# Kernel optimization log

Measured on AMD Instinct MI355X. Metric: run time of the kernel, lower is better.

## Reference

```python
import jax, jax.numpy as jnp
import numpy as np

TEMPERATURE = 0.07
NORM_EPS = 1e-12   # F.normalize eps
LOG_EPS = 1e-08


def setup_inputs() -> dict:
    key = jax.random.key(0)
    k1, k2 = jax.random.split(key)
    N, D, C = 8192, 512, 64
    projections = jax.random.normal(k1, (N, D), dtype=jnp.float32)
    targets = jax.random.randint(k2, (N,), 0, C, dtype=jnp.int64)
    return {"projections": projections, "targets": targets}


def reference(projections, targets):
    # L2-normalize rows (matches F.normalize: x / max(||x||, eps))
    norm = jnp.linalg.norm(projections, axis=1, keepdims=True)
    p = projections / jnp.maximum(norm, NORM_EPS)

    # [N, N] cosine similarity / temperature
    sim = jnp.matmul(p, p.T) / TEMPERATURE
    # row-max subtraction for numerical stability (gradient flows through max,
    # as in the torch original)
    sim = sim - jnp.max(sim, axis=1, keepdims=True)
    exp_sim = jnp.exp(sim)

    n = projections.shape[0]
    eye = jnp.eye(n, dtype=bool)
    mask_self = ~eye                                   # exclude self-pairs
    mask_pos = (targets[:, None] == targets[None, :]) & mask_self

    denom = jnp.sum(jnp.where(mask_self, exp_sim, 0.0), axis=1, keepdims=True)
    log_prob = sim - jnp.log(denom + LOG_EPS)

    num = jnp.sum(jnp.where(mask_pos, log_prob, 0.0), axis=1)
    cnt = jnp.sum(mask_pos, axis=1).astype(log_prob.dtype)
    # divide_no_nan: 0 where cnt == 0
    loss_per_sample = jnp.where(cnt == 0, 0.0, num / jnp.where(cnt == 0, 1.0, cnt))
    return loss_per_sample
```

## Files before the change

kernel.cpp:

```cpp
#include <hip/hip_runtime.h>
#include <hip/hip_bf16.h>
#include <math.h>

#define N_ROWS 8192
#define DIM    512
#define NCLS   64
#define BM     128
#define BK     64
#define NKT    (DIM / BK)
#define NTILE  (N_ROWS / BM)
#define NTRI   (NTILE * (NTILE + 1) / 2)
#define NSLOT  NTILE
#define M_CONST 14.285714285714286f
#define L2E     1.4426950408889634f
#define M2_CONST 20.60992915555662f
#define SCALE2  4.539815541256959f

using bf16x8 = __attribute__((ext_vector_type(8))) short;
using f32x4  = __attribute__((ext_vector_type(4))) float;

static __device__ inline unsigned short f2bf(float x) {
  unsigned u = __float_as_uint(x);
  unsigned r = u + 0x7FFFu + ((u >> 16) & 1u);
  return (unsigned short)(r >> 16);
}

__global__ __launch_bounds__(256) void normalize_rows(const float* __restrict__ proj,
                                                      unsigned short* __restrict__ outb) {
  const int row  = blockIdx.x * 4 + (threadIdx.x >> 6);
  const int lane = threadIdx.x & 63;
  const float4* src = (const float4*)(proj + (size_t)row * DIM);
  float4 a = src[lane * 2];
  float4 b = src[lane * 2 + 1];
  float ss = a.x*a.x + a.y*a.y + a.z*a.z + a.w*a.w
           + b.x*b.x + b.y*b.y + b.z*b.z + b.w*b.w;
#pragma unroll
  for (int off = 1; off < 64; off <<= 1) ss += __shfl_xor(ss, off);
  const float scale = SCALE2 / fmaxf(sqrtf(ss), 1e-12f);
  float v[8] = {a.x, a.y, a.z, a.w, b.x, b.y, b.z, b.w};
  unsigned short h[8];
#pragma unroll
  for (int i = 0; i < 8; ++i) h[i] = f2bf(v[i] * scale);
  uint4 packed;
  packed.x = (unsigned)h[0] | ((unsigned)h[1] << 16);
  packed.y = (unsigned)h[2] | ((unsigned)h[3] << 16);
  packed.z = (unsigned)h[4] | ((unsigned)h[5] << 16);
  packed.w = (unsigned)h[6] | ((unsigned)h[7] << 16);
  *(uint4*)(outb + (size_t)row * DIM + lane * 8) = packed;
}

__global__ __launch_bounds__(1024) void class_hist(const int* __restrict__ tgt,
                                                   int* __restrict__ hist) {
  __shared__ int h[16][NCLS];
  const int wid = threadIdx.x >> 6;
  const int lane = threadIdx.x & 63;
  if (lane < NCLS) h[wid][lane] = 0;
  __syncthreads();
  for (int i = threadIdx.x; i < N_ROWS; i += 1024) atomicAdd(&h[wid][tgt[i]], 1);
  __syncthreads();
  if (threadIdx.x < NCLS) {
    int s = 0;
#pragma unroll
    for (int w = 0; w < 16; ++w) s += h[w][threadIdx.x];
    hist[threadIdx.x] = s;
  }
}

__global__ __launch_bounds__(512, 4) void supcon_tile(const unsigned short* __restrict__ p16,
                                                      const int* __restrict__ tgt,
                                                      float* __restrict__ dpart,
                                                      float* __restrict__ spart) {
  const int logical = ((int)blockIdx.x & 7) * (NTRI / 8) + ((int)blockIdx.x >> 3);
  int rem = logical, br = 0;
  while (rem >= NTILE - br) { rem -= NTILE - br; ++br; }
  const int bc = br + rem;

  __shared__ short As[2][BM * BK];
  __shared__ short Bs[2][BM * BK];
  __shared__ int   tgr[BM], tgc[BM];
  __shared__ float redE[4][BM], redS[4][BM];
  __shared__ float redEc[2][BM], redSc[2][BM];

  const int tid  = threadIdx.x;
  const int lane = tid & 63;
  const int wid  = tid >> 6;
  const int wm = wid >> 2, wn = wid & 3;
  const int lhi = lane >> 4, llo = lane & 15;

  const size_t rowA0 = (size_t)br * BM;
  const size_t rowB0 = (size_t)bc * BM;

#define STAGE(BUF, KT) do {                                                         \
  _Pragma("unroll")                                                                 \
  for (int j = 0; j < 2; ++j) {                                                     \
    const int g  = tid + j * 512;                                                   \
    const int r  = g >> 3, gp = g & 7;                                              \
    const int gl = gp ^ (r & 7);                                                    \
    const unsigned short* sA = p16 + (rowA0 + r) * DIM + (KT) * BK + gl * 8;        \
    const unsigned short* sB = p16 + (rowB0 + r) * DIM + (KT) * BK + gl * 8;        \
    __builtin_amdgcn_global_load_lds((const __attribute__((address_space(1))) void*)sA, \
        (__attribute__((address_space(3))) void*)&As[BUF][g * 8], 16, 0, 0);        \
    __builtin_amdgcn_global_load_lds((const __attribute__((address_space(1))) void*)sB, \
        (__attribute__((address_space(3))) void*)&Bs[BUF][g * 8], 16, 0, 0);        \
  }                                                                                 \
} while (0)

  STAGE(0, 0);
  if (tid < BM)            tgr[tid] = tgt[br * BM + tid];
  else if (tid < 2 * BM)   tgc[tid - BM] = tgt[bc * BM + (tid - BM)];

  f32x4 zero = {0.f, 0.f, 0.f, 0.f};
  f32x4 acc[4][2];
#pragma unroll
  for (int i = 0; i < 4; ++i)
#pragma unroll
    for (int j = 0; j < 2; ++j) acc[i][j] = zero;

  __syncthreads();

#pragma unroll
  for (int kt = 0; kt < NKT; ++kt) {
    const int cur = kt & 1, nxt = cur ^ 1;

    if (kt > 0) {
      __builtin_amdgcn_s_barrier();
      __builtin_amdgcn_sched_barrier(0);
    }
    if (kt + 1 < NKT) {
      STAGE(nxt, kt + 1);
      asm volatile("s_waitcnt vmcnt(4)" ::: "memory");
    } else {
      asm volatile("s_waitcnt vmcnt(0)" ::: "memory");
    }
    __builtin_amdgcn_sched_barrier(0);
    __builtin_amdgcn_s_barrier();
    __builtin_amdgcn_sched_barrier(0);

#pragma unroll
    for (int ks = 0; ks < 2; ++ks) {
      bf16x8 af[4], bfr[2];
#pragma unroll
      for (int mi = 0; mi < 4; ++mi) {
        const int Ra = wm * 64 + mi * 16 + llo;
        af[mi] = *(const bf16x8*)&As[cur][Ra * BK + (((ks * 4 + lhi) ^ (Ra & 7)) * 8)];
      }
#pragma unroll
      for (int ni = 0; ni < 2; ++ni) {
        const int Rb = wn * 32 + ni * 16 + llo;
        bfr[ni] = *(const bf16x8*)&Bs[cur][Rb * BK + (((ks * 4 + lhi) ^ (Rb & 7)) * 8)];
      }
#pragma unroll
      for (int mi = 0; mi < 4; ++mi)
#pragma unroll
        for (int ni = 0; ni < 2; ++ni)
          acc[mi][ni] = __builtin_amdgcn_mfma_f32_16x16x32_bf16(af[mi], bfr[ni], acc[mi][ni], 0, 0, 0);
    }
  }
#undef STAGE

  const bool diag = (br == bc);
  const int tc0 = tgc[wn * 32 + llo];
  const int tc1 = tgc[wn * 32 + 16 + llo];
  float ecol[2] = {0.f, 0.f};
  float scol[2] = {0.f, 0.f};

#pragma unroll
  for (int mi = 0; mi < 4; ++mi) {
#pragma unroll
    for (int rg = 0; rg < 4; ++rg) {
      const int rin  = wm * 64 + mi * 16 + lhi * 4 + rg;
      const int trow = tgr[rin];
      float esum = 0.f, ssum = 0.f;
#pragma unroll
      for (int ni = 0; ni < 2; ++ni) {
        const int cin = wn * 32 + ni * 16 + llo;
        const float x = acc[mi][ni][rg];
        const bool self = diag && (rin == cin);
        const float e = self ? 0.f : __builtin_amdgcn_exp2f(x - M2_CONST);
        const bool pos = (!self) && (trow == (ni ? tc1 : tc0));
        const float sv = pos ? x : 0.f;
        esum += e;  ssum += sv;
        ecol[ni] += e;  scol[ni] += sv;
      }
#pragma unroll
      for (int off = 1; off < 16; off <<= 1) {
        esum += __shfl_xor(esum, off);
        ssum += __shfl_xor(ssum, off);
      }
      if (llo == 0) { redE[wn][rin] = esum; redS[wn][rin] = ssum; }
    }
  }
  if (!diag) {
#pragma unroll
    for (int ni = 0; ni < 2; ++ni) {
      float ec = ecol[ni], sc = scol[ni];
      ec += __shfl_xor(ec, 16); ec += __shfl_xor(ec, 32);
      sc += __shfl_xor(sc, 16); sc += __shfl_xor(sc, 32);
      if (lhi == 0) {
        redEc[wm][wn * 32 + ni * 16 + llo] = ec;
        redSc[wm][wn * 32 + ni * 16 + llo] = sc;
      }
    }
  }
  __syncthreads();

  if (tid < BM) {
    const float e = redE[0][tid] + redE[1][tid] + redE[2][tid] + redE[3][tid];
    const float s = redS[0][tid] + redS[1][tid] + redS[2][tid] + redS[3][tid];
    dpart[(size_t)bc * N_ROWS + rowA0 + tid] = e;
    spart[(size_t)bc * N_ROWS + rowA0 + tid] = s;
  } else if (tid < 2 * BM && !diag) {
    const int c = tid - BM;
    dpart[(size_t)br * N_ROWS + rowB0 + c] = redEc[0][c] + redEc[1][c];
    spart[(size_t)br * N_ROWS + rowB0 + c] = redSc[0][c] + redSc[1][c];
  }
}

__global__ __launch_bounds__(256) void combine_loss(const float* __restrict__ dpart,
                                                    const float* __restrict__ spart,
                                                    const int* __restrict__ tgt,
                                                    const int* __restrict__ hist,
                                                    float* __restrict__ out) {
  __shared__ float dsh[4][64], ssh[4][64];
  const int lane = threadIdx.x & 63;
  const int g    = threadIdx.x >> 6;
  const int r    = blockIdx.x * 64 + lane;
  float d = 0.f, s = 0.f;
  for (int k = g * (NSLOT / 4); k < (g + 1) * (NSLOT / 4); ++k) {
    d += dpart[(size_t)k * N_ROWS + r];
    s += spart[(size_t)k * N_ROWS + r];
  }
  dsh[g][lane] = d; ssh[g][lane] = s;
  __syncthreads();
  if (g == 0) {
    d = dsh[0][lane] + dsh[1][lane] + dsh[2][lane] + dsh[3][lane];
    s = ssh[0][lane] + ssh[1][lane] + ssh[2][lane] + ssh[3][lane];
    const int cnt = hist[tgt[r]] - 1;
    out[r] = (cnt > 0) ? (s / (L2E * (float)cnt) - M_CONST - logf(d + 1e-8f)) : 0.f;
  }
}

extern "C" void kernel_launch(void* const* d_in, const int* in_sizes, int n_in,
                              void* d_out, int out_size, void* d_ws, size_t ws_size,
                              hipStream_t stream) {
  const float* proj = (const float*)d_in[0];
  const int*   tgt  = (const int*)d_in[1];
  float* out = (float*)d_out;

  char* ws = (char*)d_ws;
  unsigned short* p16  = (unsigned short*)ws;
  float* dpart = (float*)(ws + (size_t)8  * 1024 * 1024);
  float* spart = (float*)(ws + (size_t)10 * 1024 * 1024);
  int*   hist  = (int*)(ws + (size_t)12 * 1024 * 1024);

  normalize_rows<<<N_ROWS / 4, 256, 0, stream>>>(proj, p16);
  class_hist<<<1, 1024, 0, stream>>>(tgt, hist);
  supcon_tile<<<NTRI, 512, 0, stream>>>(p16, tgt, dpart, spart);
  combine_loss<<<N_ROWS / 64, 256, 0, stream>>>(dpart, spart, tgt, hist, out);
}
```

Before: 91.70 us.

## Enlarge similarity tile to 256 with 1024-thread blocks and fuse histogram into combine

Doubles the square tile of the triangular Gram-matrix kernel from 128 to 256 rows, using 16 waves per block with a 4x4 wave grid and 4x4 MFMA accumulators per wave. The aim is more reuse of each loaded operand and far fewer tiles and partial sums. The separate class-histogram launch is removed; each combine block now rebuilds the 64-bin histogram in shared memory. In exchange, the larger LDS footprint allows only about one block per CU, leaves fewer blocks (528) with an uneven last wave, and repeats the histogram work in every combine block.

```diff
diff --git a/kernel.cpp b/kernel.cpp
--- a/kernel.cpp
+++ b/kernel.cpp
@@ -5,7 +5,7 @@
 #define N_ROWS 8192
 #define DIM    512
 #define NCLS   64
-#define BM     128
+#define BM     256
 #define BK     64
 #define NKT    (DIM / BK)
 #define NTILE  (N_ROWS / BM)
@@ -49,27 +49,10 @@
   *(uint4*)(outb + (size_t)row * DIM + lane * 8) = packed;
 }
 
-__global__ __launch_bounds__(1024) void class_hist(const int* __restrict__ tgt,
-                                                   int* __restrict__ hist) {
-  __shared__ int h[16][NCLS];
-  const int wid = threadIdx.x >> 6;
-  const int lane = threadIdx.x & 63;
-  if (lane < NCLS) h[wid][lane] = 0;
-  __syncthreads();
-  for (int i = threadIdx.x; i < N_ROWS; i += 1024) atomicAdd(&h[wid][tgt[i]], 1);
-  __syncthreads();
-  if (threadIdx.x < NCLS) {
-    int s = 0;
-#pragma unroll
-    for (int w = 0; w < 16; ++w) s += h[w][threadIdx.x];
-    hist[threadIdx.x] = s;
-  }
-}
-
-__global__ __launch_bounds__(512, 4) void supcon_tile(const unsigned short* __restrict__ p16,
-                                                      const int* __restrict__ tgt,
-                                                      float* __restrict__ dpart,
-                                                      float* __restrict__ spart) {
+__global__ __launch_bounds__(1024, 4) void supcon_tile(const unsigned short* __restrict__ p16,
+                                                       const int* __restrict__ tgt,
+                                                       float* __restrict__ dpart,
+                                                       float* __restrict__ spart) {
   const int logical = ((int)blockIdx.x & 7) * (NTRI / 8) + ((int)blockIdx.x >> 3);
   int rem = logical, br = 0;
   while (rem >= NTILE - br) { rem -= NTILE - br; ++br; }
@@ -79,7 +62,7 @@
   __shared__ short Bs[2][BM * BK];
   __shared__ int   tgr[BM], tgc[BM];
   __shared__ float redE[4][BM], redS[4][BM];
-  __shared__ float redEc[2][BM], redSc[2][BM];
+  __shared__ float redEc[4][BM], redSc[4][BM];
 
   const int tid  = threadIdx.x;
   const int lane = tid & 63;
@@ -93,7 +76,7 @@
 #define STAGE(BUF, KT) do {                                                         \
   _Pragma("unroll")                                                                 \
   for (int j = 0; j < 2; ++j) {                                                     \
-    const int g  = tid + j * 512;                                                   \
+    const int g  = tid + j * 1024;                                                  \
     const int r  = g >> 3, gp = g & 7;                                              \
     const int gl = gp ^ (r & 7);                                                    \
     const unsigned short* sA = p16 + (rowA0 + r) * DIM + (KT) * BK + gl * 8;        \
@@ -110,11 +93,11 @@
   else if (tid < 2 * BM)   tgc[tid - BM] = tgt[bc * BM + (tid - BM)];
 
   f32x4 zero = {0.f, 0.f, 0.f, 0.f};
-  f32x4 acc[4][2];
+  f32x4 acc[4][4];
 #pragma unroll
   for (int i = 0; i < 4; ++i)
 #pragma unroll
-    for (int j = 0; j < 2; ++j) acc[i][j] = zero;
+    for (int j = 0; j < 4; ++j) acc[i][j] = zero;
 
   __syncthreads();
 
@@ -138,31 +121,32 @@
 
 #pragma unroll
     for (int ks = 0; ks < 2; ++ks) {
-      bf16x8 af[4], bfr[2];
+      bf16x8 af[4], bfr[4];
 #pragma unroll
       for (int mi = 0; mi < 4; ++mi) {
         const int Ra = wm * 64 + mi * 16 + llo;
         af[mi] = *(const bf16x8*)&As[cur][Ra * BK + (((ks * 4 + lhi) ^ (Ra & 7)) * 8)];
       }
 #pragma unroll
-      for (int ni = 0; ni < 2; ++ni) {
-        const int Rb = wn * 32 + ni * 16 + llo;
+      for (int ni = 0; ni < 4; ++ni) {
+        const int Rb = wn * 64 + ni * 16 + llo;
         bfr[ni] = *(const bf16x8*)&Bs[cur][Rb * BK + (((ks * 4 + lhi) ^ (Rb & 7)) * 8)];
       }
 #pragma unroll
       for (int mi = 0; mi < 4; ++mi)
 #pragma unroll
-        for (int ni = 0; ni < 2; ++ni)
+        for (int ni = 0; ni < 4; ++ni)
           acc[mi][ni] = __builtin_amdgcn_mfma_f32_16x16x32_bf16(af[mi], bfr[ni], acc[mi][ni], 0, 0, 0);
     }
   }
 #undef STAGE
 
   const bool diag = (br == bc);
-  const int tc0 = tgc[wn * 32 + llo];
-  const int tc1 = tgc[wn * 32 + 16 + llo];
-  float ecol[2] = {0.f, 0.f};
-  float scol[2] = {0.f, 0.f};
+  int tc[4];
+#pragma unroll
+  for (int ni = 0; ni < 4; ++ni) tc[ni] = tgc[wn * 64 + ni * 16 + llo];
+  float ecol[4] = {0.f, 0.f, 0.f, 0.f};
+  float scol[4] = {0.f, 0.f, 0.f, 0.f};
 
 #pragma unroll
   for (int mi = 0; mi < 4; ++mi) {
@@ -172,12 +156,12 @@
       const int trow = tgr[rin];
       float esum = 0.f, ssum = 0.f;
 #pragma unroll
-      for (int ni = 0; ni < 2; ++ni) {
-        const int cin = wn * 32 + ni * 16 + llo;
+      for (int ni = 0; ni < 4; ++ni) {
+        const int cin = wn * 64 + ni * 16 + llo;
         const float x = acc[mi][ni][rg];
         const bool self = diag && (rin == cin);
         const float e = self ? 0.f : __builtin_amdgcn_exp2f(x - M2_CONST);
-        const bool pos = (!self) && (trow == (ni ? tc1 : tc0));
+        const bool pos = (!self) && (trow == tc[ni]);
         const float sv = pos ? x : 0.f;
         esum += e;  ssum += sv;
         ecol[ni] += e;  scol[ni] += sv;
@@ -192,13 +176,13 @@
   }
   if (!diag) {
 #pragma unroll
-    for (int ni = 0; ni < 2; ++ni) {
+    for (int ni = 0; ni < 4; ++ni) {
       float ec = ecol[ni], sc = scol[ni];
       ec += __shfl_xor(ec, 16); ec += __shfl_xor(ec, 32);
       sc += __shfl_xor(sc, 16); sc += __shfl_xor(sc, 32);
       if (lhi == 0) {
-        redEc[wm][wn * 32 + ni * 16 + llo] = ec;
-        redSc[wm][wn * 32 + ni * 16 + llo] = sc;
+        redEc[wm][wn * 64 + ni * 16 + llo] = ec;
+        redSc[wm][wn * 64 + ni * 16 + llo] = sc;
       }
     }
   }
@@ -211,20 +195,26 @@
     spart[(size_t)bc * N_ROWS + rowA0 + tid] = s;
   } else if (tid < 2 * BM && !diag) {
     const int c = tid - BM;
-    dpart[(size_t)br * N_ROWS + rowB0 + c] = redEc[0][c] + redEc[1][c];
-    spart[(size_t)br * N_ROWS + rowB0 + c] = redSc[0][c] + redSc[1][c];
+    dpart[(size_t)br * N_ROWS + rowB0 + c] = redEc[0][c] + redEc[1][c] + redEc[2][c] + redEc[3][c];
+    spart[(size_t)br * N_ROWS + rowB0 + c] = redSc[0][c] + redSc[1][c] + redSc[2][c] + redSc[3][c];
   }
 }
 
 __global__ __launch_bounds__(256) void combine_loss(const float* __restrict__ dpart,
                                                     const float* __restrict__ spart,
                                                     const int* __restrict__ tgt,
-                                                    const int* __restrict__ hist,
                                                     float* __restrict__ out) {
   __shared__ float dsh[4][64], ssh[4][64];
-  const int lane = threadIdx.x & 63;
-  const int g    = threadIdx.x >> 6;
+  __shared__ int   hloc[NCLS];
+  const int tid  = threadIdx.x;
+  const int lane = tid & 63;
+  const int g    = tid >> 6;
   const int r    = blockIdx.x * 64 + lane;
+
+  if (tid < NCLS) hloc[tid] = 0;
+  __syncthreads();
+  for (int i = tid; i < N_ROWS; i += 256) atomicAdd(&hloc[tgt[i]], 1);
+
   float d = 0.f, s = 0.f;
   for (int k = g * (NSLOT / 4); k < (g + 1) * (NSLOT / 4); ++k) {
     d += dpart[(size_t)k * N_ROWS + r];
@@ -235,7 +225,7 @@
   if (g == 0) {
     d = dsh[0][lane] + dsh[1][lane] + dsh[2][lane] + dsh[3][lane];
     s = ssh[0][lane] + ssh[1][lane] + ssh[2][lane] + ssh[3][lane];
-    const int cnt = hist[tgt[r]] - 1;
+    const int cnt = hloc[tgt[r]] - 1;
     out[r] = (cnt > 0) ? (s / (L2E * (float)cnt) - M_CONST - logf(d + 1e-8f)) : 0.f;
   }
 }
@@ -249,12 +239,10 @@
 
   char* ws = (char*)d_ws;
   unsigned short* p16  = (unsigned short*)ws;
-  float* dpart = (float*)(ws + (size_t)8  * 1024 * 1024);
-  float* spart = (float*)(ws + (size_t)10 * 1024 * 1024);
-  int*   hist  = (int*)(ws + (size_t)12 * 1024 * 1024);
+  float* dpart = (float*)(ws + (size_t)8 * 1024 * 1024);
+  float* spart = (float*)(ws + (size_t)9 * 1024 * 1024);
 
   normalize_rows<<<N_ROWS / 4, 256, 0, stream>>>(proj, p16);
-  class_hist<<<1, 1024, 0, stream>>>(tgt, hist);
-  supcon_tile<<<NTRI, 512, 0, stream>>>(p16, tgt, dpart, spart);
-  combine_loss<<<N_ROWS / 64, 256, 0, stream>>>(dpart, spart, tgt, hist, out);
-}
+  supcon_tile<<<NTRI, 1024, 0, stream>>>(p16, tgt, dpart, spart);
+  combine_loss<<<N_ROWS / 64, 256, 0, stream>>>(dpart, spart, tgt, out);
+}
```

After: 99.21 us. 1.08x slower.
